# Performance work log

Measured on AMD Instinct MI355X. Metric: run time of the kernel, lower is better.

## Reference

```python
import jax, jax.numpy as jnp
import numpy as np

K = 20          # num neighbors (init kwarg k)
BN_EPS = 1e-5   # PyTorch BatchNorm default eps


def setup_inputs() -> dict:
    key = jax.random.key(0)
    k1, k2 = jax.random.split(key, 2)
    x = jax.random.normal(k1, (8, 64, 4096), dtype=jnp.float32)       # (b, d, n)
    w = jax.random.normal(k2, (64, 128), dtype=jnp.float32) * 0.05    # Conv2d 1x1: (out=64, in=2*64)
    gamma = jnp.ones((64,), jnp.float32)    # BatchNorm1d weight
    beta = jnp.zeros((64,), jnp.float32)    # BatchNorm1d bias
    return {"x": x, "w": w, "gamma": gamma, "beta": beta}


def reference(x, w, gamma, beta):
    # x: (b, d, n)
    xt = jnp.swapaxes(x, 1, 2)                       # (b, n, d)
    # kNN via pairwise squared euclidean distance (same ordering as torch.cdist)
    sq = jnp.sum(xt * xt, axis=-1)                   # (b, n)
    d2 = sq[:, :, None] + sq[:, None, :] - 2.0 * jnp.einsum('bnd,bmd->bnm', xt, xt)
    _, idx = jax.lax.top_k(-d2, K)                   # (b, n, K) smallest distances
    # gather neighbor features: (b, n, K, d)
    nb = jax.vmap(lambda pts, i: pts[i])(xt, idx)
    ctr = xt[:, :, None, :]                          # (b, n, 1, d)
    # edge feature = concat([neighbor - x, x]) -> (b, n, K, 2d)
    feat = jnp.concatenate([nb - ctr, jnp.broadcast_to(ctr, nb.shape)], axis=-1)
    # 1x1 conv (no bias) then max over neighbors
    h = jnp.max(jnp.einsum('bnkc,oc->bnko', feat, w), axis=2)   # (b, n, out)
    # BatchNorm1d (training mode: batch statistics over (b, n), biased var)
    mean = jnp.mean(h, axis=(0, 1))
    var = jnp.mean((h - mean) ** 2, axis=(0, 1))
    hn = (h - mean) / jnp.sqrt(var + BN_EPS) * gamma + beta
    out = jax.nn.gelu(hn, approximate=False)         # exact GELU (PyTorch default)
    return jnp.swapaxes(out, 1, 2)                   # (b, out, n)
```

## Files before the change

kernel.cpp:

```cpp
#include <hip/hip_runtime.h>

#define BIGF 3.402823466e38f

typedef __attribute__((ext_vector_type(8))) short bf16x8;
typedef __attribute__((ext_vector_type(4))) float f32x4;

__device__ __forceinline__ void gload_lds16u(const unsigned short* g, unsigned short* lds) {
  __builtin_amdgcn_global_load_lds((const __attribute__((address_space(1))) void*)g,
                                   (__attribute__((address_space(3))) void*)lds, 16, 0, 0);
}

__device__ __forceinline__ unsigned short bf16_rne(float f) {
  unsigned int u = __float_as_uint(f);
  return (unsigned short)((u + 0x7fffu + ((u >> 16) & 1u)) >> 16);
}

__global__ __launch_bounds__(256) void k1_pre(const float* __restrict__ x, const float* __restrict__ w,
                                              float* __restrict__ sq, float* __restrict__ y,
                                              float* __restrict__ delta, unsigned short* __restrict__ xhl) {
  __shared__ __align__(16) float xt[64][68];
  __shared__ __align__(16) float ws[128][64];
  const int t = threadIdx.x;
  const int bid = blockIdx.x;
  const int b = bid >> 6;
  const int n0 = (bid & 63) << 6;
  const float* xb = x + (size_t)b * 64 * 4096;

#pragma unroll
  for (int rep = 0; rep < 16; ++rep) {
    int id = rep * 256 + t;
    int d = id >> 6, n = id & 63;
    xt[n][d] = xb[(size_t)d * 4096 + n0 + n];
  }
#pragma unroll
  for (int rep = 0; rep < 32; ++rep) {
    int id = rep * 256 + t;
    int u = id >> 6, dd = id & 63;
    ws[u][dd] = w[(u & 63) * 128 + ((u >> 6) << 6) + dd];
  }
  __syncthreads();

  {
    const int p = t >> 2;
    const int cg = t & 3;
    uint4* orow = (uint4*)xhl + ((size_t)(b << 12) + n0 + p) * 16;
#pragma unroll
    for (int cc = 0; cc < 4; ++cc) {
      const int c = cg * 4 + cc;
      const int kb = (c & 7) * 8;
      const bool lohalf = (c >= 8);
      unsigned int pk[4];
#pragma unroll
      for (int j2 = 0; j2 < 4; ++j2) {
        unsigned short u0, u1;
#pragma unroll
        for (int e = 0; e < 2; ++e) {
          const float xv = xt[p][kb + j2 * 2 + e];
          unsigned short h = bf16_rne(xv);
          unsigned short r;
          if (!lohalf) r = h;
          else r = bf16_rne(xv - __uint_as_float(((unsigned int)h) << 16));
          if (e == 0) u0 = r; else u1 = r;
        }
        pk[j2] = (unsigned int)u0 | ((unsigned int)u1 << 16);
      }
      uint4 v;
      v.x = pk[0]; v.y = pk[1]; v.z = pk[2]; v.w = pk[3];
      orow[c ^ (p & 7)] = v;
    }
  }

  const int p = t & 63;
  const int oc = t >> 6;
  float accy[16], accz[16];
#pragma unroll
  for (int j = 0; j < 16; ++j) { accy[j] = 0.f; accz[j] = 0.f; }

#pragma unroll 4
  for (int d4 = 0; d4 < 16; ++d4) {
    const float4 xv = *(const float4*)&xt[p][d4 * 4];
#pragma unroll
    for (int j = 0; j < 16; ++j) {
      const int o = oc * 16 + j;
      const float4 wy = *(const float4*)&ws[o][d4 * 4];
      const float4 wz = *(const float4*)&ws[o + 64][d4 * 4];
      accy[j] = fmaf(xv.x, wy.x, fmaf(xv.y, wy.y, fmaf(xv.z, wy.z, fmaf(xv.w, wy.w, accy[j]))));
      accz[j] = fmaf(xv.x, wz.x, fmaf(xv.y, wz.y, fmaf(xv.z, wz.z, fmaf(xv.w, wz.w, accz[j]))));
    }
  }

  if (oc == 0) {
    float s = 0.f;
#pragma unroll
    for (int d4 = 0; d4 < 16; ++d4) {
      const float4 v = *(const float4*)&xt[p][d4 * 4];
      s = fmaf(v.x, v.x, fmaf(v.y, v.y, fmaf(v.z, v.z, fmaf(v.w, v.w, s))));
    }
    sq[b * 4096 + n0 + p] = s;
  }

  const size_t row = ((size_t)b * 4096 + n0 + p) * 64 + oc * 16;
#pragma unroll
  for (int j4 = 0; j4 < 4; ++j4) {
    float4 yv = make_float4(accy[j4 * 4], accy[j4 * 4 + 1], accy[j4 * 4 + 2], accy[j4 * 4 + 3]);
    float4 dv = make_float4(accz[j4 * 4] - accy[j4 * 4], accz[j4 * 4 + 1] - accy[j4 * 4 + 1],
                            accz[j4 * 4 + 2] - accy[j4 * 4 + 2], accz[j4 * 4 + 3] - accy[j4 * 4 + 3]);
    *(float4*)&y[row + j4 * 4] = yv;
    *(float4*)&delta[row + j4 * 4] = dv;
  }
}

__global__ __launch_bounds__(256, 3) void k2_knn(const unsigned short* __restrict__ xhl,
                                                 const float* __restrict__ sq,
                                                 int* __restrict__ idx_out) {
  __shared__ __align__(16) float smem[12800];
  const int t = threadIdx.x;
  const int lane = t & 63;
  const int w = t >> 6;
  float* BsW = smem + (w << 11);
  uint2* bufL = (uint2*)(smem + 8192) + ((w << 6) + lane) * 9;

  const int bid = blockIdx.x;
  const int b = bid >> 6;
  const int n0 = (bid & 63) << 6;
  const int pn = lane & 15, q = lane >> 4;

  const unsigned short* xr = xhl + ((size_t)(b << 12)) * 128;
  const float* sqb = sq + (b << 12);

  {
    unsigned short* asu = (unsigned short*)smem;
#pragma unroll
    for (int qq = 0; qq < 4; ++qq) {
      const int kk = w * 4 + qq;
      gload_lds16u(xr + (size_t)n0 * 128 + kk * 512 + lane * 8, asu + kk * 512);
    }
  }
  __syncthreads();

  bf16x8 bfr[4][4];
  {
    const uint4* As4 = (const uint4*)smem;
#pragma unroll
    for (int nt = 0; nt < 4; ++nt)
#pragma unroll
      for (int j = 0; j < 4; ++j)
        bfr[nt][j] = *reinterpret_cast<const bf16x8*>(&As4[((nt << 4) + pn) * 16 + (((j << 2) + q) ^ (pn & 7))]);
  }
  __syncthreads();

  float kd[20];
  int ki[20];
#pragma unroll
  for (int s = 0; s < 20; ++s) { kd[s] = BIGF; ki[s] = -1; }
  const float sqn = sqb[n0 + lane];
  const int myn = lane;
  const int swz = myn & 7;
  int cnt = 0;
  float taup = BIGF;

  auto ins = [&](float vd, int vi) {
#pragma unroll
    for (int s = 0; s < 20; ++s) {
      const float od = kd[s];
      const int oi = ki[s];
      const bool lt = vd < od;
      kd[s] = lt ? vd : od;
      ki[s] = lt ? vi : oi;
      vd = lt ? od : vd;
      vi = lt ? oi : vi;
    }
  };

  auto drain = [&]() {
#pragma unroll 1
    for (int j = 0; j < 8; ++j) {
      if (!__any(j < cnt)) break;
      if (j < cnt) {
        const uint2 e = bufL[j];
        const float dv = sqn + __uint_as_float(e.x);
        if (dv < kd[19]) ins(dv, (int)e.y);
      }
    }
    cnt = 0;
    taup = kd[19] - sqn;
  };

  const f32x4 zero4 = {0.f, 0.f, 0.f, 0.f};
  f32x4 acc[4][2];
#pragma unroll
  for (int nt = 0; nt < 4; ++nt) { acc[nt][0] = zero4; acc[nt][1] = zero4; }

  for (int kt = 0; kt < 32; ++kt) {
    const int mbase = (w + 4 * kt) << 5;
    {
      unsigned short* bsu = (unsigned short*)BsW;
      const unsigned short* src = xr + (size_t)mbase * 128;
#pragma unroll
      for (int k = 0; k < 8; ++k) gload_lds16u(src + k * 512 + lane * 8, bsu + k * 512);
    }
    const f32x4 sqm0 = *(const f32x4*)&sqb[mbase + (q << 2)];
    const f32x4 sqm1 = *(const f32x4*)&sqb[mbase + 16 + (q << 2)];
    __builtin_amdgcn_s_waitcnt(0x0F70);

#pragma unroll
    for (int mt = 0; mt < 2; ++mt) {
      bf16x8 afr[4];
#pragma unroll
      for (int j = 0; j < 4; ++j)
        afr[j] = *reinterpret_cast<const bf16x8*>(&((const uint4*)BsW)[((mt << 4) + pn) * 16 + (((j << 2) + q) ^ (pn & 7))]);
#pragma unroll
      for (int nt = 0; nt < 4; ++nt) {
        f32x4 a = acc[nt][mt];
        a = __builtin_amdgcn_mfma_f32_16x16x32_bf16(afr[0], bfr[nt][0], a, 0, 0, 0);
        a = __builtin_amdgcn_mfma_f32_16x16x32_bf16(afr[1], bfr[nt][1], a, 0, 0, 0);
        a = __builtin_amdgcn_mfma_f32_16x16x32_bf16(afr[0], bfr[nt][2], a, 0, 0, 0);
        a = __builtin_amdgcn_mfma_f32_16x16x32_bf16(afr[1], bfr[nt][3], a, 0, 0, 0);
        a = __builtin_amdgcn_mfma_f32_16x16x32_bf16(afr[2], bfr[nt][0], a, 0, 0, 0);
        a = __builtin_amdgcn_mfma_f32_16x16x32_bf16(afr[3], bfr[nt][1], a, 0, 0, 0);
        acc[nt][mt] = a;
      }
    }

#pragma unroll
    for (int nt = 0; nt < 4; ++nt) {
#pragma unroll
      for (int mt = 0; mt < 2; ++mt) {
        const int n = (nt << 4) + pn;
        const int g = (mt << 2) + q;
        const int pc = g ^ (n & 7);
        const f32x4 sv = mt ? sqm1 : sqm0;
        f32x4 dv = sv - 2.0f * acc[nt][mt];
        *(f32x4*)&BsW[(n << 5) + (pc << 2)] = dv;
        acc[nt][mt] = zero4;
      }
    }

#pragma unroll 1
    for (int cc = 0; cc < 8; ++cc) {
      const float4 v = *(const float4*)&BsW[(myn << 5) + ((cc ^ swz) << 2)];
      const int mb = mbase + (cc << 2);
      const float mn = fminf(fminf(v.x, v.y), fminf(v.z, v.w));
      if (mn < taup) {
        if (v.x < taup) { bufL[cnt] = make_uint2(__float_as_uint(v.x), (unsigned)mb); cnt++; }
        if (v.y < taup) { bufL[cnt] = make_uint2(__float_as_uint(v.y), (unsigned)(mb + 1)); cnt++; }
        if (v.z < taup) { bufL[cnt] = make_uint2(__float_as_uint(v.z), (unsigned)(mb + 2)); cnt++; }
        if (v.w < taup) { bufL[cnt] = make_uint2(__float_as_uint(v.w), (unsigned)(mb + 3)); cnt++; }
      }
      if (__any(cnt > 4)) drain();
    }
  }
  drain();

  __syncthreads();
  float* pf = smem;
  int* pi = (int*)(smem + 5120);
#pragma unroll
  for (int s = 0; s < 20; ++s) {
    pf[(w * 20 + s) * 64 + lane] = kd[s];
    pi[(w * 20 + s) * 64 + lane] = ki[s];
  }
  __syncthreads();
  if (w == 0) {
    auto insTie = [&](float vd, int vi) {
#pragma unroll
      for (int s = 0; s < 20; ++s) {
        const float od = kd[s];
        const int oi = ki[s];
        const bool lt = (vd < od) || (vd == od && vi < oi);
        kd[s] = lt ? vd : od;
        ki[s] = lt ? vi : oi;
        vd = lt ? od : vd;
        vi = lt ? oi : vi;
      }
    };
    for (int ww = 1; ww < 4; ++ww) {
#pragma unroll 1
      for (int s = 0; s < 20; ++s) {
        const float dv = pf[(ww * 20 + s) * 64 + lane];
        const int iv = pi[(ww * 20 + s) * 64 + lane];
        if (dv < kd[19] || (dv == kd[19] && iv < ki[19])) insTie(dv, iv);
      }
    }
    int* orow = idx_out + ((size_t)(b << 12) + n0 + lane) * 20;
#pragma unroll
    for (int s = 0; s < 20; ++s) orow[s] = ki[s];
  }
}

__global__ __launch_bounds__(256) void k3_gather(const float* __restrict__ y,
                                                 const float* __restrict__ delta,
                                                 const int* __restrict__ idx,
                                                 float* __restrict__ h,
                                                 float* __restrict__ sums,
                                                 float* __restrict__ sumsq) {
  __shared__ float r1[16][64], r2[16][64];
  const int t = threadIdx.x;
  const int cg = t & 15;
  const int pw = t >> 4;
  const int blk = blockIdx.x;
  float4 s1 = make_float4(0.f, 0.f, 0.f, 0.f), s2 = s1;
#pragma unroll 1
  for (int pp = 0; pp < 2; ++pp) {
    const int ng = blk * 32 + pp * 16 + pw;
    const int b = ng >> 12;
    const int* row = idx + (size_t)ng * 20;
    float4 mx = make_float4(-BIGF, -BIGF, -BIGF, -BIGF);
#pragma unroll
    for (int kk = 0; kk < 20; ++kk) {
      const int nbr = row[kk];
      const float4 v = *(const float4*)&y[(((size_t)(b << 12)) + nbr) * 64 + cg * 4];
      mx.x = fmaxf(mx.x, v.x); mx.y = fmaxf(mx.y, v.y);
      mx.z = fmaxf(mx.z, v.z); mx.w = fmaxf(mx.w, v.w);
    }
    const float4 dl = *(const float4*)&delta[(size_t)ng * 64 + cg * 4];
    float4 hv = make_float4(mx.x + dl.x, mx.y + dl.y, mx.z + dl.z, mx.w + dl.w);
    *(float4*)&h[(size_t)ng * 64 + cg * 4] = hv;
    s1.x += hv.x; s1.y += hv.y; s1.z += hv.z; s1.w += hv.w;
    s2.x += hv.x * hv.x; s2.y += hv.y * hv.y; s2.z += hv.z * hv.z; s2.w += hv.w * hv.w;
  }
  *(float4*)&r1[pw][cg * 4] = s1;
  *(float4*)&r2[pw][cg * 4] = s2;
  __syncthreads();
  if (t < 64) {
    float a = 0.f, c = 0.f;
#pragma unroll
    for (int i = 0; i < 16; ++i) { a += r1[i][t]; c += r2[i][t]; }
    atomicAdd(&sums[t], a);
    atomicAdd(&sumsq[t], c);
  }
}

__global__ __launch_bounds__(256) void k4_bn(const float* __restrict__ h,
                                             const float* __restrict__ sums,
                                             const float* __restrict__ sumsq,
                                             const float* __restrict__ gamma,
                                             const float* __restrict__ beta,
                                             float* __restrict__ out) {
  __shared__ float tile[64][65];
  const int bid = blockIdx.x;
  const int b = bid >> 6;
  const int n0 = (bid & 63) << 6;
  const int t = threadIdx.x;
  const int o = t & 63;
#pragma unroll
  for (int it = 0; it < 16; ++it) {
    const int n = (t >> 6) * 16 + it;
    tile[n][o] = h[(((size_t)b << 12) + n0 + n) * 64 + o];
  }
  __syncthreads();
  const int j = t & 63;
#pragma unroll
  for (int it = 0; it < 16; ++it) {
    const int oo = (t >> 6) * 16 + it;
    const float mean = sums[oo] * (1.0f / 32768.0f);
    const float var = sumsq[oo] * (1.0f / 32768.0f) - mean * mean;
    const float sc = gamma[oo] / sqrtf(var + 1e-5f);
    const float hv = tile[j][oo];
    const float hn = (hv - mean) * sc + beta[oo];
    const float g = 0.5f * hn * (1.0f + erff(hn * 0.70710678118654752f));
    out[((size_t)(b * 64 + oo)) * 4096 + n0 + j] = g;
  }
}

extern "C" void kernel_launch(void* const* d_in, const int* in_sizes, int n_in,
                              void* d_out, int out_size, void* d_ws, size_t ws_size,
                              hipStream_t stream) {
  const float* x = (const float*)d_in[0];
  const float* w = (const float*)d_in[1];
  const float* gamma = (const float*)d_in[2];
  const float* beta = (const float*)d_in[3];
  float* out = (float*)d_out;

  float* sq_ws = (float*)d_ws;
  float* y_ws = sq_ws + 32768;
  float* delta_ws = y_ws + 2097152;
  float* h_ws = delta_ws + 2097152;
  int* idx_ws = (int*)(h_ws + 2097152);
  float* sums = (float*)(idx_ws + 655360);
  float* sumsq = sums + 64;
  unsigned short* xhl = (unsigned short*)h_ws;

  hipMemsetAsync(sums, 0, 2 * 64 * sizeof(float), stream);
  k1_pre<<<512, 256, 0, stream>>>(x, w, sq_ws, y_ws, delta_ws, xhl);
  k2_knn<<<512, 256, 0, stream>>>(xhl, sq_ws, idx_ws);
  k3_gather<<<1024, 256, 0, stream>>>(y_ws, delta_ws, idx_ws, h_ws, sums, sumsq);
  k4_bn<<<512, 256, 0, stream>>>(h_ws, sums, sumsq, gamma, beta, out);
}
```

Measured before the change: 376.1 us.

## Split kNN candidate scan across eight waves with tree merge of per-wave top-k

The kNN kernel now runs 512 threads per block (8 waves) instead of 4, so each wave scans half as many candidate tiles. The per-lane candidate buffer moves to a lane-strided LDS queue that is drained after every chunk, with a fully unrolled 4-entry drain. The final merge of per-wave top-20 lists becomes a three-level tree reduction, replacing the serial merge of three lists by wave 0. This adds LDS (80 KB per block), more barriers and more frequent drains, which may limit occupancy.

```diff
diff --git a/kernel.cpp b/kernel.cpp
--- a/kernel.cpp
+++ b/kernel.cpp
@@ -110,15 +110,15 @@
   }
 }
 
-__global__ __launch_bounds__(256, 3) void k2_knn(const unsigned short* __restrict__ xhl,
+__global__ __launch_bounds__(512, 4) void k2_knn(const unsigned short* __restrict__ xhl,
                                                  const float* __restrict__ sq,
                                                  int* __restrict__ idx_out) {
-  __shared__ __align__(16) float smem[12800];
+  __shared__ __align__(16) float smem[20480];
   const int t = threadIdx.x;
   const int lane = t & 63;
   const int w = t >> 6;
   float* BsW = smem + (w << 11);
-  uint2* bufL = (uint2*)(smem + 8192) + ((w << 6) + lane) * 9;
+  uint2* bufQ = (uint2*)(smem + 16384);
 
   const int bid = blockIdx.x;
   const int b = bid >> 6;
@@ -131,8 +131,8 @@
   {
     unsigned short* asu = (unsigned short*)smem;
 #pragma unroll
-    for (int qq = 0; qq < 4; ++qq) {
-      const int kk = w * 4 + qq;
+    for (int qq = 0; qq < 2; ++qq) {
+      const int kk = w * 2 + qq;
       gload_lds16u(xr + (size_t)n0 * 128 + kk * 512 + lane * 8, asu + kk * 512);
     }
   }
@@ -173,11 +173,11 @@
   };
 
   auto drain = [&]() {
-#pragma unroll 1
-    for (int j = 0; j < 8; ++j) {
+#pragma unroll
+    for (int j = 0; j < 4; ++j) {
       if (!__any(j < cnt)) break;
       if (j < cnt) {
-        const uint2 e = bufL[j];
+        const uint2 e = bufQ[((w << 2) + j) * 64 + lane];
         const float dv = sqn + __uint_as_float(e.x);
         if (dv < kd[19]) ins(dv, (int)e.y);
       }
@@ -191,8 +191,8 @@
 #pragma unroll
   for (int nt = 0; nt < 4; ++nt) { acc[nt][0] = zero4; acc[nt][1] = zero4; }
 
-  for (int kt = 0; kt < 32; ++kt) {
-    const int mbase = (w + 4 * kt) << 5;
+  for (int kt = 0; kt < 16; ++kt) {
+    const int mbase = (w + 8 * kt) << 5;
     {
       unsigned short* bsu = (unsigned short*)BsW;
       const unsigned short* src = xr + (size_t)mbase * 128;
@@ -242,46 +242,59 @@
       const int mb = mbase + (cc << 2);
       const float mn = fminf(fminf(v.x, v.y), fminf(v.z, v.w));
       if (mn < taup) {
-        if (v.x < taup) { bufL[cnt] = make_uint2(__float_as_uint(v.x), (unsigned)mb); cnt++; }
-        if (v.y < taup) { bufL[cnt] = make_uint2(__float_as_uint(v.y), (unsigned)(mb + 1)); cnt++; }
-        if (v.z < taup) { bufL[cnt] = make_uint2(__float_as_uint(v.z), (unsigned)(mb + 2)); cnt++; }
-        if (v.w < taup) { bufL[cnt] = make_uint2(__float_as_uint(v.w), (unsigned)(mb + 3)); cnt++; }
+        if (v.x < taup) { bufQ[((w << 2) + cnt) * 64 + lane] = make_uint2(__float_as_uint(v.x), (unsigned)mb); cnt++; }
+        if (v.y < taup) { bufQ[((w << 2) + cnt) * 64 + lane] = make_uint2(__float_as_uint(v.y), (unsigned)(mb + 1)); cnt++; }
+        if (v.z < taup) { bufQ[((w << 2) + cnt) * 64 + lane] = make_uint2(__float_as_uint(v.z), (unsigned)(mb + 2)); cnt++; }
+        if (v.w < taup) { bufQ[((w << 2) + cnt) * 64 + lane] = make_uint2(__float_as_uint(v.w), (unsigned)(mb + 3)); cnt++; }
       }
-      if (__any(cnt > 4)) drain();
-    }
-  }
-  drain();
+      if (__any(cnt > 0)) drain();
+    }
+  }
 
   __syncthreads();
   float* pf = smem;
   int* pi = (int*)(smem + 5120);
-#pragma unroll
-  for (int s = 0; s < 20; ++s) {
-    pf[(w * 20 + s) * 64 + lane] = kd[s];
-    pi[(w * 20 + s) * 64 + lane] = ki[s];
-  }
+
+  auto insTie = [&](float vd, int vi) {
+#pragma unroll
+    for (int s = 0; s < 20; ++s) {
+      const float od = kd[s];
+      const int oi = ki[s];
+      const bool lt = (vd < od) || (vd == od && vi < oi);
+      kd[s] = lt ? vd : od;
+      ki[s] = lt ? vi : oi;
+      vd = lt ? od : vd;
+      vi = lt ? oi : vi;
+    }
+  };
+  auto mergeSlot = [&](int slot) {
+#pragma unroll 1
+    for (int s = 0; s < 20; ++s) {
+      const float dv = pf[(slot * 20 + s) * 64 + lane];
+      const int iv = pi[(slot * 20 + s) * 64 + lane];
+      if (dv < kd[19] || (dv == kd[19] && iv < ki[19])) insTie(dv, iv);
+    }
+  };
+  auto publish = [&](int slot) {
+#pragma unroll
+    for (int s = 0; s < 20; ++s) {
+      pf[(slot * 20 + s) * 64 + lane] = kd[s];
+      pi[(slot * 20 + s) * 64 + lane] = ki[s];
+    }
+  };
+
+  if (w >= 4) publish(w - 4);
+  __syncthreads();
+  if (w < 4) mergeSlot(w);
+  __syncthreads();
+  if (w == 2 || w == 3) publish(w - 2);
+  __syncthreads();
+  if (w < 2) mergeSlot(w);
+  __syncthreads();
+  if (w == 1) publish(0);
   __syncthreads();
   if (w == 0) {
-    auto insTie = [&](float vd, int vi) {
-#pragma unroll
-      for (int s = 0; s < 20; ++s) {
-        const float od = kd[s];
-        const int oi = ki[s];
-        const bool lt = (vd < od) || (vd == od && vi < oi);
-        kd[s] = lt ? vd : od;
-        ki[s] = lt ? vi : oi;
-        vd = lt ? od : vd;
-        vi = lt ? oi : vi;
-      }
-    };
-    for (int ww = 1; ww < 4; ++ww) {
-#pragma unroll 1
-      for (int s = 0; s < 20; ++s) {
-        const float dv = pf[(ww * 20 + s) * 64 + lane];
-        const int iv = pi[(ww * 20 + s) * 64 + lane];
-        if (dv < kd[19] || (dv == kd[19] && iv < ki[19])) insTie(dv, iv);
-      }
-    }
+    mergeSlot(0);
     int* orow = idx_out + ((size_t)(b << 12) + n0 + lane) * 20;
 #pragma unroll
     for (int s = 0; s < 20; ++s) orow[s] = ki[s];
@@ -383,7 +396,7 @@
 
   hipMemsetAsync(sums, 0, 2 * 64 * sizeof(float), stream);
   k1_pre<<<512, 256, 0, stream>>>(x, w, sq_ws, y_ws, delta_ws, xhl);
-  k2_knn<<<512, 256, 0, stream>>>(xhl, sq_ws, idx_ws);
+  k2_knn<<<512, 512, 0, stream>>>(xhl, sq_ws, idx_ws);
   k3_gather<<<1024, 256, 0, stream>>>(y_ws, delta_ws, idx_ws, h_ws, sums, sumsq);
   k4_bn<<<512, 256, 0, stream>>>(h_ws, sums, sumsq, gamma, beta, out);
 }
```

Result: slower. 540.2 us (+43.6%).
